# Optimization experiments

Measured on AMD Instinct MI355X. Metric: run time of the kernel, lower is better.

The kernel has to match this reference:

```python
import jax, jax.numpy as jnp
import numpy as np

EPS = 1e-5

def _rmsnorm(x, w):
    # Faithful to the repo's rms_norm: divides by sqrt(SUM of squares + eps)
    # (the .mean(-1) in the original acts on a size-1 dim and is a no-op).
    rms = jnp.sqrt(jnp.sum(x * x, axis=-1, keepdims=True) + EPS)
    return (x / rms) * w

def _conv2d(x, w, b):
    # x: (N, C=m, H=L, W=2*d_model), w: (O, I, 3, 3), padding=1 -> SAME
    y = jax.lax.conv_general_dilated(
        x, w, window_strides=(1, 1), padding='SAME',
        dimension_numbers=('NCHW', 'OIHW', 'NCHW'))
    return y + b[None, :, None, None]

def _ssm(x, fc1_W, fc1_b, fc2_W, fc2_b, A):
    # x: (b, m, l, d) with d = 2*d_model; state dim n = 128
    Bm = x @ fc2_W.T + fc2_b                       # (b,m,l,n); C = fc2(x) as well -> identical
    delta = jax.nn.softplus(x @ fc1_W.T + fc1_b)   # (b,m,l,d)
    dA = jnp.exp(jnp.einsum('bmld,dn->bmldn', delta, A))   # (b,m,l,d,n)
    dB = jnp.einsum('bmld,bmln->bmldn', delta, Bm)         # (b,m,l,d,n)
    h_new = dA + x[..., None] * dB                 # h is initialized to ones and never updated
    return jnp.einsum('bmln,bmldn->bmld', Bm, h_new)

def setup_inputs() -> dict:
    key = jax.random.key(0)
    ks = jax.random.split(key, 16)
    B, M, L, D = 1, 2, 256, 256
    D2, S = 2 * D, 128
    def rn(k, shape, scale=0.02):
        return jax.random.normal(k, shape, jnp.float32) * scale
    return {
        'x': jax.random.normal(ks[0], (B, M, L, D), jnp.float32),
        'mouth': jax.random.normal(ks[1], (B, M, L, D), jnp.float32),
        'norm_w': jnp.ones((D,), jnp.float32),
        'inp_W': rn(ks[2], (D2, D)), 'inp_b': rn(ks[3], (D2,)),
        'out_W': rn(ks[4], (D, D2)), 'out_b': jnp.ones((D,), jnp.float32),  # bias init 1.0
        'Dlin_W': rn(ks[5], (D2, D)), 'Dlin_b': rn(ks[6], (D2,)),
        'conv_W': rn(ks[7], (M, M, 3, 3), 0.1), 'conv_b': rn(ks[8], (M,)),
        'fc1_W': rn(ks[9], (D2, D2)), 'fc1_b': rn(ks[10], (D2,)),
        'fc2_W': rn(ks[11], (S, D2)), 'fc2_b': rn(ks[12], (S,)),
        'A': rn(ks[13], (D2, S), 0.05),
    }

def reference(x, mouth, norm_w, inp_W, inp_b, out_W, out_b, Dlin_W, Dlin_b,
              conv_W, conv_b, fc1_W, fc1_b, fc2_W, fc2_b, A):
    x_n = _rmsnorm(x, norm_w)
    m_n = _rmsnorm(mouth, norm_w)
    x_p = x_n @ inp_W.T + inp_b        # (B,M,L,2D)
    m_p = m_n @ inp_W.T + inp_b
    x_c = jax.nn.silu(_conv2d(x_p, conv_W, conv_b))
    m_c = jax.nn.silu(_conv2d(m_p, conv_W, conv_b))
    x_s = jax.nn.silu(_ssm(x_c, fc1_W, fc1_b, fc2_W, fc2_b, A))
    m_s = jax.nn.silu(_ssm(m_c, fc1_W, fc1_b, fc2_W, fc2_b, A))
    res = jax.nn.silu(x_n @ Dlin_W.T + Dlin_b)   # D(x) uses the normed x
    comb = x_s * res + m_s * res
    return comb @ out_W.T + out_b
```

## Files before the change

### kernel.cpp

```cpp
#include <hip/hip_runtime.h>
#include <hip/hip_bf16.h>
#include <math.h>


#define D_   256
#define D2_  512
#define S_   128

__device__ __forceinline__ float silu_f(float v) {
    return v / (1.f + __expf(-v));
}
__device__ __forceinline__ float softplus_f(float v) {
    return fmaxf(v, 0.f) + log1pf(__expf(-fabsf(v)));
}

template<bool NORM, int ACT1, int ACT2>
__global__ __launch_bounds__(256) void gemm_dual_k(
        const float* __restrict__ A0, const float* __restrict__ A1,
        const float* __restrict__ nw,
        const float* __restrict__ W1, const float* __restrict__ bias1,
        float* __restrict__ O1, int nct1, int ldo1, int n1,
        const float* __restrict__ W2, const float* __restrict__ bias2,
        float* __restrict__ O2, int nct2, int ldo2, int K) {
    __shared__ float As[2][32][36];
    __shared__ float Ws[2][32][68];
    const int b = blockIdx.x;
    const float *W, *bias; float* O; int ldo, act, rt, ct;
    if (b < n1) { W = W1; bias = bias1; O = O1; ldo = ldo1; act = ACT1; rt = b / nct1; ct = b % nct1; }
    else { int bb = b - n1; W = W2; bias = bias2; O = O2; ldo = ldo2; act = ACT2; rt = bb / nct2; ct = bb % nct2; }
    const int r0 = rt * 32, c0 = ct * 64;
    const int t = threadIdx.x;
    const int sr = t >> 3;
    const int sk = (t & 7) << 2;
    const int rowA = r0 + sr;
    const float* rowbase = (rowA < 512) ? (A0 + (size_t)rowA * K)
                                        : (A1 + (size_t)(rowA - 512) * K);
    float ascale = 1.f;
    if (NORM) {
        const int j = t & 7;
        float ssum = 0.f;
        const float* rp = rowbase + j * 32;
#pragma unroll
        for (int q = 0; q < 8; ++q) {
            float4 v = *(const float4*)(rp + q * 4);
            ssum += v.x * v.x + v.y * v.y + v.z * v.z + v.w * v.w;
        }
        ssum += __shfl_xor(ssum, 1);
        ssum += __shfl_xor(ssum, 2);
        ssum += __shfl_xor(ssum, 4);
        ascale = 1.f / sqrtf(ssum + 1e-5f);
    }
    const float* Abase  = rowbase + sk;
    const float* W1base = W + (size_t)(c0 + sr) * K + sk;
    const float* W2base = W + (size_t)(c0 + 32 + sr) * K + sk;
    float4 areg  = *(const float4*)Abase;
    float4 w1reg = *(const float4*)W1base;
    float4 w2reg = *(const float4*)W2base;
    float4 nwreg = NORM ? *(const float4*)(nw + sk) : make_float4(0.f, 0.f, 0.f, 0.f);
    const int tr = (t >> 5) << 2;
    const int tc = (t & 31) << 1;
    float acc[4][2] = {};
    const int nch = K >> 5;
    for (int ch = 0; ch < nch; ++ch) {
        const int p = ch & 1;
        float4 a = areg;
        if (NORM) {
            a.x *= ascale * nwreg.x; a.y *= ascale * nwreg.y;
            a.z *= ascale * nwreg.z; a.w *= ascale * nwreg.w;
        }
        As[p][sk + 0][sr] = a.x;  As[p][sk + 1][sr] = a.y;
        As[p][sk + 2][sr] = a.z;  As[p][sk + 3][sr] = a.w;
        Ws[p][sk + 0][sr] = w1reg.x;  Ws[p][sk + 1][sr] = w1reg.y;
        Ws[p][sk + 2][sr] = w1reg.z;  Ws[p][sk + 3][sr] = w1reg.w;
        Ws[p][sk + 0][sr + 32] = w2reg.x;  Ws[p][sk + 1][sr + 32] = w2reg.y;
        Ws[p][sk + 2][sr + 32] = w2reg.z;  Ws[p][sk + 3][sr + 32] = w2reg.w;
        __syncthreads();
        if (ch + 1 < nch) {
            const int ko = (ch + 1) << 5;
            areg  = *(const float4*)(Abase + ko);
            w1reg = *(const float4*)(W1base + ko);
            w2reg = *(const float4*)(W2base + ko);
            if (NORM) nwreg = *(const float4*)(nw + ko + sk);
        }
#pragma unroll
        for (int kk = 0; kk < 32; ++kk) {
            const float4 a4 = *(const float4*)&As[p][kk][tr];
            const float2 w2 = *(const float2*)&Ws[p][kk][tc];
            acc[0][0] = fmaf(a4.x, w2.x, acc[0][0]); acc[0][1] = fmaf(a4.x, w2.y, acc[0][1]);
            acc[1][0] = fmaf(a4.y, w2.x, acc[1][0]); acc[1][1] = fmaf(a4.y, w2.y, acc[1][1]);
            acc[2][0] = fmaf(a4.z, w2.x, acc[2][0]); acc[2][1] = fmaf(a4.z, w2.y, acc[2][1]);
            acc[3][0] = fmaf(a4.w, w2.x, acc[3][0]); acc[3][1] = fmaf(a4.w, w2.y, acc[3][1]);
        }
    }
    const float2 bv = *(const float2*)(bias + c0 + tc);
#pragma unroll
    for (int i = 0; i < 4; ++i) {
        float vx = acc[i][0] + bv.x, vy = acc[i][1] + bv.y;
        if (act == 1)      { vx = silu_f(vx);     vy = silu_f(vy); }
        else if (act == 2) { vx = softplus_f(vx); vy = softplus_f(vy); }
        *(float2*)(O + (size_t)(r0 + tr + i) * ldo + c0 + tc) = make_float2(vx, vy);
    }
}

__global__ void conv_silu_k(const float* __restrict__ xp, const float* __restrict__ cW,
                            const float* __restrict__ cb, float* __restrict__ xc) {
    int idx = blockIdx.x * blockDim.x + threadIdx.x;
    int w = idx & 511;
    int l = (idx >> 9) & 255;
    int o = (idx >> 17) & 1;
    int t = idx >> 18;
    float acc = cb[o];
#pragma unroll
    for (int i = 0; i < 2; ++i) {
        const float* base = xp + (size_t)((t * 2 + i) * 256) * 512;
#pragma unroll
        for (int dh = -1; dh <= 1; ++dh) {
            int ll = l + dh;
            if (ll < 0 || ll > 255) continue;
#pragma unroll
            for (int dw = -1; dw <= 1; ++dw) {
                int ww = w + dw;
                if (ww < 0 || ww > 511) continue;
                acc += base[(size_t)ll * 512 + ww] * cW[((o * 2 + i) * 3 + (dh + 1)) * 3 + (dw + 1)];
            }
        }
    }
    xc[idx] = silu_f(acc);
}

__global__ __launch_bounds__(512) void ssm_out_k(
        const float* __restrict__ xc, const float* __restrict__ delta,
        const float* __restrict__ Bm, const float* __restrict__ A,
        const float* __restrict__ res, const float* __restrict__ outW,
        const float* __restrict__ outb, float* __restrict__ out) {
    __shared__ float Bms[2][2][S_];
    __shared__ float combs[2][D2_];
    __shared__ float red[8];
    const int tid = threadIdx.x;
    const int m  = blockIdx.x >> 7;
    const int l0 = (blockIdx.x & 127) << 1;

    {
        const int g = tid >> 7;
        const int tt = g >> 1, lr = g & 1, n = tid & 127;
        const int rg = tt * 512 + m * 256 + l0 + lr;
        float bv = Bm[(size_t)rg * S_ + n];
        Bms[tt][lr][n] = bv;
        float sq = bv * bv;
        for (int off = 32; off; off >>= 1) sq += __shfl_xor(sq, off);
        if ((tid & 63) == 0) red[tid >> 6] = sq;
    }
    __syncthreads();
    {
        const int d = tid;
        float s2[2][2];
#pragma unroll
        for (int g = 0; g < 4; ++g) s2[g >> 1][g & 1] = red[2 * g] + red[2 * g + 1];
        float dl[2][2], xcv[2][2], rsv[2];
#pragma unroll
        for (int tt = 0; tt < 2; ++tt)
#pragma unroll
            for (int lr = 0; lr < 2; ++lr) {
                const size_t r = (size_t)(tt * 512 + m * 256 + l0 + lr);
                dl[tt][lr]  = delta[r * D2_ + d];
                xcv[tt][lr] = xc[r * D2_ + d];
            }
        rsv[0] = res[(size_t)(m * 256 + l0) * D2_ + d];
        rsv[1] = res[(size_t)(m * 256 + l0 + 1) * D2_ + d];
        float accs[2][2] = {};
        const float4* arow = (const float4*)(A + (size_t)d * S_);
        for (int k4 = 0; k4 < 32; ++k4) {
            float4 a4 = arow[k4];
            const int n = k4 * 4;
#pragma unroll
            for (int cmp = 0; cmp < 4; ++cmp) {
                float a = (cmp == 0) ? a4.x : (cmp == 1) ? a4.y : (cmp == 2) ? a4.z : a4.w;
#pragma unroll
                for (int tt = 0; tt < 2; ++tt)
#pragma unroll
                    for (int lr = 0; lr < 2; ++lr)
                        accs[tt][lr] += Bms[tt][lr][n + cmp] * __expf(dl[tt][lr] * a);
            }
        }
#pragma unroll
        for (int lr = 0; lr < 2; ++lr) {
            float sx = accs[0][lr] + xcv[0][lr] * dl[0][lr] * s2[0][lr];
            float sm = accs[1][lr] + xcv[1][lr] * dl[1][lr] * s2[1][lr];
            combs[lr][d] = (silu_f(sx) + silu_f(sm)) * rsv[lr];
        }
    }
    __syncthreads();
    {
        const int wv = tid >> 6, lane = tid & 63;
        const int j = lane & 15, cg = lane >> 4;
#pragma unroll
        for (int rnd = 0; rnd < 8; ++rnd) {
            const int c = wv * 32 + rnd * 4 + cg;
            const float4* wrow = (const float4*)(outW + (size_t)c * D2_);
            float a0 = 0.f, a1 = 0.f;
#pragma unroll
            for (int it = 0; it < 8; ++it) {
                const int k = it * 64 + j * 4;
                float4 w4 = wrow[it * 16 + j];
                a0 += w4.x * combs[0][k] + w4.y * combs[0][k + 1]
                    + w4.z * combs[0][k + 2] + w4.w * combs[0][k + 3];
                a1 += w4.x * combs[1][k] + w4.y * combs[1][k + 1]
                    + w4.z * combs[1][k + 2] + w4.w * combs[1][k + 3];
            }
            a0 += __shfl_xor(a0, 1); a0 += __shfl_xor(a0, 2);
            a0 += __shfl_xor(a0, 4); a0 += __shfl_xor(a0, 8);
            a1 += __shfl_xor(a1, 1); a1 += __shfl_xor(a1, 2);
            a1 += __shfl_xor(a1, 4); a1 += __shfl_xor(a1, 8);
            if (j == 0) {
                const float b = outb[c];
                out[(size_t)(m * 256 + l0)     * D_ + c] = a0 + b;
                out[(size_t)(m * 256 + l0 + 1) * D_ + c] = a1 + b;
            }
        }
    }
}

extern "C" void kernel_launch(void* const* d_in, const int* in_sizes, int n_in,
                              void* d_out, int out_size, void* d_ws, size_t ws_size,
                              hipStream_t stream) {
    const float* x      = (const float*)d_in[0];
    const float* mouth  = (const float*)d_in[1];
    const float* norm_w = (const float*)d_in[2];
    const float* inp_W  = (const float*)d_in[3];
    const float* inp_b  = (const float*)d_in[4];
    const float* out_W  = (const float*)d_in[5];
    const float* out_b  = (const float*)d_in[6];
    const float* Dlin_W = (const float*)d_in[7];
    const float* Dlin_b = (const float*)d_in[8];
    const float* conv_W = (const float*)d_in[9];
    const float* conv_b = (const float*)d_in[10];
    const float* fc1_W  = (const float*)d_in[11];
    const float* fc1_b  = (const float*)d_in[12];
    const float* fc2_W  = (const float*)d_in[13];
    const float* fc2_b  = (const float*)d_in[14];
    const float* A      = (const float*)d_in[15];

    float* ws    = (float*)d_ws;
    float* xp    = ws;
    float* xc    = xp + 1024 * 512;
    float* res   = xc + 1024 * 512;
    float* Bmb   = res + 512 * 512;
    float* delta = xp;
    float* out   = (float*)d_out;

    gemm_dual_k<true, 0, 1><<<384, 256, 0, stream>>>(
        x, mouth, norm_w,
        inp_W, inp_b, xp, 8, 512, 256,
        Dlin_W, Dlin_b, res, 8, 512, 256);
    conv_silu_k<<<2048, 256, 0, stream>>>(xp, conv_W, conv_b, xc);
    gemm_dual_k<false, 2, 0><<<320, 256, 0, stream>>>(
        xc, xc + (size_t)512 * 512, nullptr,
        fc1_W, fc1_b, delta, 8, 512, 256,
        fc2_W, fc2_b, Bmb, 2, 128, 512);
    ssm_out_k<<<256, 512, 0, stream>>>(xc, delta, Bmb, A, res,
                                       out_W, out_b, out);
}
```

Measured before the change: 161.1 us.

## Merge four kernel launches into one cooperative persistent kernel with grid syncs

```diff
diff --git a/kernel.cpp b/kernel.cpp
--- a/kernel.cpp
+++ b/kernel.cpp
@@ -1,11 +1,10 @@
 #include <hip/hip_runtime.h>
+#include <hip/hip_cooperative_groups.h>
 #include <hip/hip_bf16.h>
 #include <math.h>
 
-
-#define D_   256
-#define D2_  512
-#define S_   128
+namespace cg = cooperative_groups;
+
 
 __device__ __forceinline__ float silu_f(float v) {
     return v / (1.f + __expf(-v));
@@ -14,22 +13,13 @@
     return fmaxf(v, 0.f) + log1pf(__expf(-fabsf(v)));
 }
 
-template<bool NORM, int ACT1, int ACT2>
-__global__ __launch_bounds__(256) void gemm_dual_k(
-        const float* __restrict__ A0, const float* __restrict__ A1,
-        const float* __restrict__ nw,
-        const float* __restrict__ W1, const float* __restrict__ bias1,
-        float* __restrict__ O1, int nct1, int ldo1, int n1,
-        const float* __restrict__ W2, const float* __restrict__ bias2,
-        float* __restrict__ O2, int nct2, int ldo2, int K) {
-    __shared__ float As[2][32][36];
-    __shared__ float Ws[2][32][68];
-    const int b = blockIdx.x;
-    const float *W, *bias; float* O; int ldo, act, rt, ct;
-    if (b < n1) { W = W1; bias = bias1; O = O1; ldo = ldo1; act = ACT1; rt = b / nct1; ct = b % nct1; }
-    else { int bb = b - n1; W = W2; bias = bias2; O = O2; ldo = ldo2; act = ACT2; rt = bb / nct2; ct = bb % nct2; }
+__device__ void gemm_tile(const float* __restrict__ A0, const float* __restrict__ A1,
+                          const float* __restrict__ nw, bool NORM,
+                          const float* __restrict__ W, const float* __restrict__ bias,
+                          float* __restrict__ O, int ldo, int act,
+                          int rt, int ct, int K,
+                          float* AsB, float* WsB, int t, bool active) {
     const int r0 = rt * 32, c0 = ct * 64;
-    const int t = threadIdx.x;
     const int sr = t >> 3;
     const int sk = (t & 7) << 2;
     const int rowA = r0 + sr;
@@ -37,9 +27,8 @@
                                         : (A1 + (size_t)(rowA - 512) * K);
     float ascale = 1.f;
     if (NORM) {
-        const int j = t & 7;
         float ssum = 0.f;
-        const float* rp = rowbase + j * 32;
+        const float* rp = rowbase + (t & 7) * 32;
 #pragma unroll
         for (int q = 0; q < 8; ++q) {
             float4 v = *(const float4*)(rp + q * 4);
@@ -50,12 +39,12 @@
         ssum += __shfl_xor(ssum, 4);
         ascale = 1.f / sqrtf(ssum + 1e-5f);
     }
-    const float* Abase  = rowbase + sk;
-    const float* W1base = W + (size_t)(c0 + sr) * K + sk;
-    const float* W2base = W + (size_t)(c0 + 32 + sr) * K + sk;
-    float4 areg  = *(const float4*)Abase;
-    float4 w1reg = *(const float4*)W1base;
-    float4 w2reg = *(const float4*)W2base;
+    const float* Abase = rowbase + sk;
+    const float* W1b = W + (size_t)(c0 + sr) * K + sk;
+    const float* W2b = W + (size_t)(c0 + 32 + sr) * K + sk;
+    float4 areg = *(const float4*)Abase;
+    float4 w1   = *(const float4*)W1b;
+    float4 w2   = *(const float4*)W2b;
     float4 nwreg = NORM ? *(const float4*)(nw + sk) : make_float4(0.f, 0.f, 0.f, 0.f);
     const int tr = (t >> 5) << 2;
     const int tc = (t & 31) << 1;
@@ -68,153 +57,205 @@
             a.x *= ascale * nwreg.x; a.y *= ascale * nwreg.y;
             a.z *= ascale * nwreg.z; a.w *= ascale * nwreg.w;
         }
-        As[p][sk + 0][sr] = a.x;  As[p][sk + 1][sr] = a.y;
-        As[p][sk + 2][sr] = a.z;  As[p][sk + 3][sr] = a.w;
-        Ws[p][sk + 0][sr] = w1reg.x;  Ws[p][sk + 1][sr] = w1reg.y;
-        Ws[p][sk + 2][sr] = w1reg.z;  Ws[p][sk + 3][sr] = w1reg.w;
-        Ws[p][sk + 0][sr + 32] = w2reg.x;  Ws[p][sk + 1][sr + 32] = w2reg.y;
-        Ws[p][sk + 2][sr + 32] = w2reg.z;  Ws[p][sk + 3][sr + 32] = w2reg.w;
+        AsB[p * 1152 + (sk + 0) * 36 + sr] = a.x;
+        AsB[p * 1152 + (sk + 1) * 36 + sr] = a.y;
+        AsB[p * 1152 + (sk + 2) * 36 + sr] = a.z;
+        AsB[p * 1152 + (sk + 3) * 36 + sr] = a.w;
+        WsB[p * 2176 + (sk + 0) * 68 + sr] = w1.x;
+        WsB[p * 2176 + (sk + 1) * 68 + sr] = w1.y;
+        WsB[p * 2176 + (sk + 2) * 68 + sr] = w1.z;
+        WsB[p * 2176 + (sk + 3) * 68 + sr] = w1.w;
+        WsB[p * 2176 + (sk + 0) * 68 + sr + 32] = w2.x;
+        WsB[p * 2176 + (sk + 1) * 68 + sr + 32] = w2.y;
+        WsB[p * 2176 + (sk + 2) * 68 + sr + 32] = w2.z;
+        WsB[p * 2176 + (sk + 3) * 68 + sr + 32] = w2.w;
         __syncthreads();
         if (ch + 1 < nch) {
             const int ko = (ch + 1) << 5;
-            areg  = *(const float4*)(Abase + ko);
-            w1reg = *(const float4*)(W1base + ko);
-            w2reg = *(const float4*)(W2base + ko);
+            areg = *(const float4*)(Abase + ko);
+            w1   = *(const float4*)(W1b + ko);
+            w2   = *(const float4*)(W2b + ko);
             if (NORM) nwreg = *(const float4*)(nw + ko + sk);
         }
 #pragma unroll
         for (int kk = 0; kk < 32; ++kk) {
-            const float4 a4 = *(const float4*)&As[p][kk][tr];
-            const float2 w2 = *(const float2*)&Ws[p][kk][tc];
-            acc[0][0] = fmaf(a4.x, w2.x, acc[0][0]); acc[0][1] = fmaf(a4.x, w2.y, acc[0][1]);
-            acc[1][0] = fmaf(a4.y, w2.x, acc[1][0]); acc[1][1] = fmaf(a4.y, w2.y, acc[1][1]);
-            acc[2][0] = fmaf(a4.z, w2.x, acc[2][0]); acc[2][1] = fmaf(a4.z, w2.y, acc[2][1]);
-            acc[3][0] = fmaf(a4.w, w2.x, acc[3][0]); acc[3][1] = fmaf(a4.w, w2.y, acc[3][1]);
-        }
-    }
-    const float2 bv = *(const float2*)(bias + c0 + tc);
-#pragma unroll
-    for (int i = 0; i < 4; ++i) {
-        float vx = acc[i][0] + bv.x, vy = acc[i][1] + bv.y;
-        if (act == 1)      { vx = silu_f(vx);     vy = silu_f(vy); }
-        else if (act == 2) { vx = softplus_f(vx); vy = softplus_f(vy); }
-        *(float2*)(O + (size_t)(r0 + tr + i) * ldo + c0 + tc) = make_float2(vx, vy);
-    }
-}
-
-__global__ void conv_silu_k(const float* __restrict__ xp, const float* __restrict__ cW,
-                            const float* __restrict__ cb, float* __restrict__ xc) {
-    int idx = blockIdx.x * blockDim.x + threadIdx.x;
-    int w = idx & 511;
-    int l = (idx >> 9) & 255;
-    int o = (idx >> 17) & 1;
-    int t = idx >> 18;
-    float acc = cb[o];
-#pragma unroll
-    for (int i = 0; i < 2; ++i) {
-        const float* base = xp + (size_t)((t * 2 + i) * 256) * 512;
-#pragma unroll
-        for (int dh = -1; dh <= 1; ++dh) {
-            int ll = l + dh;
-            if (ll < 0 || ll > 255) continue;
-#pragma unroll
-            for (int dw = -1; dw <= 1; ++dw) {
-                int ww = w + dw;
-                if (ww < 0 || ww > 511) continue;
-                acc += base[(size_t)ll * 512 + ww] * cW[((o * 2 + i) * 3 + (dh + 1)) * 3 + (dw + 1)];
+            const float4 a4 = *(const float4*)&AsB[p * 1152 + kk * 36 + tr];
+            const float2 wv = *(const float2*)&WsB[p * 2176 + kk * 68 + tc];
+            acc[0][0] = fmaf(a4.x, wv.x, acc[0][0]); acc[0][1] = fmaf(a4.x, wv.y, acc[0][1]);
+            acc[1][0] = fmaf(a4.y, wv.x, acc[1][0]); acc[1][1] = fmaf(a4.y, wv.y, acc[1][1]);
+            acc[2][0] = fmaf(a4.z, wv.x, acc[2][0]); acc[2][1] = fmaf(a4.z, wv.y, acc[2][1]);
+            acc[3][0] = fmaf(a4.w, wv.x, acc[3][0]); acc[3][1] = fmaf(a4.w, wv.y, acc[3][1]);
+        }
+    }
+    if (active) {
+        const float2 bv = *(const float2*)(bias + c0 + tc);
+#pragma unroll
+        for (int i = 0; i < 4; ++i) {
+            float vx = acc[i][0] + bv.x, vy = acc[i][1] + bv.y;
+            if (act == 1)      { vx = silu_f(vx);     vy = silu_f(vy); }
+            else if (act == 2) { vx = softplus_f(vx); vy = softplus_f(vy); }
+            *(float2*)(O + (size_t)(r0 + tr + i) * ldo + c0 + tc) = make_float2(vx, vy);
+        }
+    }
+}
+
+__global__ __launch_bounds__(512) void coop_k(
+        const float* __restrict__ x, const float* __restrict__ mouth,
+        const float* __restrict__ nw,
+        const float* __restrict__ inpW, const float* __restrict__ inpb,
+        const float* __restrict__ outW, const float* __restrict__ outb,
+        const float* __restrict__ DW,   const float* __restrict__ Db,
+        const float* __restrict__ convW, const float* __restrict__ convB,
+        const float* __restrict__ fc1W, const float* __restrict__ fc1b,
+        const float* __restrict__ fc2W, const float* __restrict__ fc2b,
+        const float* __restrict__ A,
+        float* xp, float* xc, float* res, float* Bm, float* out) {
+    __shared__ float smem[13312];
+    cg::grid_group grid = cg::this_grid();
+    const int tid  = threadIdx.x;
+    const int half = tid >> 8;
+    const int t    = tid & 255;
+    float* AsB = smem + half * 6656;
+    float* WsB = AsB + 2304;
+
+    {
+        const int job = blockIdx.x * 2 + half;
+        const bool active = job < 384;
+        const int j = active ? job : 0;
+        const bool isres = j >= 256;
+        const int jj = isres ? j - 256 : j;
+        gemm_tile(x, mouth, nw, true,
+                  isres ? DW : inpW, isres ? Db : inpb,
+                  isres ? res : xp, 512, isres ? 1 : 0,
+                  jj >> 3, jj & 7, 256, AsB, WsB, t, active);
+    }
+    grid.sync();
+    {
+#pragma unroll
+        for (int jj = 0; jj < 4; ++jj) {
+            const int idx = jj * 131072 + blockIdx.x * 512 + tid;
+            const int w = idx & 511;
+            const int l = (idx >> 9) & 255;
+            const int o = (idx >> 17) & 1;
+            const int tt = idx >> 18;
+            float acc = convB[o];
+#pragma unroll
+            for (int i = 0; i < 2; ++i) {
+                const float* base = xp + (size_t)((tt * 2 + i) * 256) * 512;
+#pragma unroll
+                for (int dh = -1; dh <= 1; ++dh) {
+                    int ll = l + dh;
+                    if (ll < 0 || ll > 255) continue;
+#pragma unroll
+                    for (int dw = -1; dw <= 1; ++dw) {
+                        int ww = w + dw;
+                        if (ww < 0 || ww > 511) continue;
+                        acc += base[(size_t)ll * 512 + ww]
+                             * convW[((o * 2 + i) * 3 + (dh + 1)) * 3 + (dw + 1)];
+                    }
+                }
             }
-        }
-    }
-    xc[idx] = silu_f(acc);
-}
-
-__global__ __launch_bounds__(512) void ssm_out_k(
-        const float* __restrict__ xc, const float* __restrict__ delta,
-        const float* __restrict__ Bm, const float* __restrict__ A,
-        const float* __restrict__ res, const float* __restrict__ outW,
-        const float* __restrict__ outb, float* __restrict__ out) {
-    __shared__ float Bms[2][2][S_];
-    __shared__ float combs[2][D2_];
-    __shared__ float red[8];
-    const int tid = threadIdx.x;
-    const int m  = blockIdx.x >> 7;
-    const int l0 = (blockIdx.x & 127) << 1;
-
+            xc[idx] = silu_f(acc);
+        }
+    }
+    grid.sync();
     {
-        const int g = tid >> 7;
-        const int tt = g >> 1, lr = g & 1, n = tid & 127;
-        const int rg = tt * 512 + m * 256 + l0 + lr;
-        float bv = Bm[(size_t)rg * S_ + n];
-        Bms[tt][lr][n] = bv;
-        float sq = bv * bv;
-        for (int off = 32; off; off >>= 1) sq += __shfl_xor(sq, off);
-        if ((tid & 63) == 0) red[tid >> 6] = sq;
-    }
-    __syncthreads();
+        const int job = blockIdx.x * 2 + half;
+        const bool active = job < 320;
+        const int j = active ? job : 0;
+        const bool isfc2 = j >= 256;
+        const int jj = isfc2 ? j - 256 : j;
+        gemm_tile(xc, xc + (size_t)512 * 512, nullptr, false,
+                  isfc2 ? fc2W : fc1W, isfc2 ? fc2b : fc1b,
+                  isfc2 ? Bm : xp, isfc2 ? 128 : 512, isfc2 ? 0 : 2,
+                  isfc2 ? (jj >> 1) : (jj >> 3), isfc2 ? (jj & 1) : (jj & 7),
+                  512, AsB, WsB, t, active);
+    }
+    grid.sync();
     {
-        const int d = tid;
-        float s2[2][2];
-#pragma unroll
-        for (int g = 0; g < 4; ++g) s2[g >> 1][g & 1] = red[2 * g] + red[2 * g + 1];
-        float dl[2][2], xcv[2][2], rsv[2];
-#pragma unroll
-        for (int tt = 0; tt < 2; ++tt)
+        float* Bms   = smem;
+        float* combs = smem + 512;
+        float* red   = smem + 1536;
+        const float* delta = xp;
+        const int m  = blockIdx.x >> 7;
+        const int l0 = (blockIdx.x & 127) << 1;
+        {
+            const int g = tid >> 7;
+            const int tt = g >> 1, lr = g & 1, n = tid & 127;
+            const int rg = tt * 512 + m * 256 + l0 + lr;
+            float bv = Bm[(size_t)rg * 128 + n];
+            Bms[g * 128 + n] = bv;
+            float sq = bv * bv;
+            for (int off = 32; off; off >>= 1) sq += __shfl_xor(sq, off);
+            if ((tid & 63) == 0) red[tid >> 6] = sq;
+        }
+        __syncthreads();
+        {
+            const int d = tid;
+            float s2[2][2];
+#pragma unroll
+            for (int g = 0; g < 4; ++g) s2[g >> 1][g & 1] = red[2 * g] + red[2 * g + 1];
+            float dl[2][2], xcv[2][2], rsv[2];
+#pragma unroll
+            for (int tt = 0; tt < 2; ++tt)
+#pragma unroll
+                for (int lr = 0; lr < 2; ++lr) {
+                    const size_t r = (size_t)(tt * 512 + m * 256 + l0 + lr);
+                    dl[tt][lr]  = delta[r * 512 + d];
+                    xcv[tt][lr] = xc[r * 512 + d];
+                }
+            rsv[0] = res[(size_t)(m * 256 + l0) * 512 + d];
+            rsv[1] = res[(size_t)(m * 256 + l0 + 1) * 512 + d];
+            float accs[2][2] = {};
+            const float4* arow = (const float4*)(A + (size_t)d * 128);
+            for (int k4 = 0; k4 < 32; ++k4) {
+                float4 a4 = arow[k4];
+                const int n = k4 * 4;
+#pragma unroll
+                for (int cmp = 0; cmp < 4; ++cmp) {
+                    float a = (cmp == 0) ? a4.x : (cmp == 1) ? a4.y : (cmp == 2) ? a4.z : a4.w;
+#pragma unroll
+                    for (int tt = 0; tt < 2; ++tt)
+#pragma unroll
+                        for (int lr = 0; lr < 2; ++lr)
+                            accs[tt][lr] += Bms[(tt * 2 + lr) * 128 + n + cmp]
+                                          * __expf(dl[tt][lr] * a);
+                }
+            }
 #pragma unroll
             for (int lr = 0; lr < 2; ++lr) {
-                const size_t r = (size_t)(tt * 512 + m * 256 + l0 + lr);
-                dl[tt][lr]  = delta[r * D2_ + d];
-                xcv[tt][lr] = xc[r * D2_ + d];
+                float sx = accs[0][lr] + xcv[0][lr] * dl[0][lr] * s2[0][lr];
+                float sm = accs[1][lr] + xcv[1][lr] * dl[1][lr] * s2[1][lr];
+                combs[lr * 512 + d] = (silu_f(sx) + silu_f(sm)) * rsv[lr];
             }
-        rsv[0] = res[(size_t)(m * 256 + l0) * D2_ + d];
-        rsv[1] = res[(size_t)(m * 256 + l0 + 1) * D2_ + d];
-        float accs[2][2] = {};
-        const float4* arow = (const float4*)(A + (size_t)d * S_);
-        for (int k4 = 0; k4 < 32; ++k4) {
-            float4 a4 = arow[k4];
-            const int n = k4 * 4;
-#pragma unroll
-            for (int cmp = 0; cmp < 4; ++cmp) {
-                float a = (cmp == 0) ? a4.x : (cmp == 1) ? a4.y : (cmp == 2) ? a4.z : a4.w;
-#pragma unroll
-                for (int tt = 0; tt < 2; ++tt)
-#pragma unroll
-                    for (int lr = 0; lr < 2; ++lr)
-                        accs[tt][lr] += Bms[tt][lr][n + cmp] * __expf(dl[tt][lr] * a);
-            }
-        }
-#pragma unroll
-        for (int lr = 0; lr < 2; ++lr) {
-            float sx = accs[0][lr] + xcv[0][lr] * dl[0][lr] * s2[0][lr];
-            float sm = accs[1][lr] + xcv[1][lr] * dl[1][lr] * s2[1][lr];
-            combs[lr][d] = (silu_f(sx) + silu_f(sm)) * rsv[lr];
-        }
-    }
-    __syncthreads();
-    {
-        const int wv = tid >> 6, lane = tid & 63;
-        const int j = lane & 15, cg = lane >> 4;
-#pragma unroll
-        for (int rnd = 0; rnd < 8; ++rnd) {
-            const int c = wv * 32 + rnd * 4 + cg;
-            const float4* wrow = (const float4*)(outW + (size_t)c * D2_);
-            float a0 = 0.f, a1 = 0.f;
-#pragma unroll
-            for (int it = 0; it < 8; ++it) {
-                const int k = it * 64 + j * 4;
-                float4 w4 = wrow[it * 16 + j];
-                a0 += w4.x * combs[0][k] + w4.y * combs[0][k + 1]
-                    + w4.z * combs[0][k + 2] + w4.w * combs[0][k + 3];
-                a1 += w4.x * combs[1][k] + w4.y * combs[1][k + 1]
-                    + w4.z * combs[1][k + 2] + w4.w * combs[1][k + 3];
-            }
-            a0 += __shfl_xor(a0, 1); a0 += __shfl_xor(a0, 2);
-            a0 += __shfl_xor(a0, 4); a0 += __shfl_xor(a0, 8);
-            a1 += __shfl_xor(a1, 1); a1 += __shfl_xor(a1, 2);
-            a1 += __shfl_xor(a1, 4); a1 += __shfl_xor(a1, 8);
-            if (j == 0) {
-                const float b = outb[c];
-                out[(size_t)(m * 256 + l0)     * D_ + c] = a0 + b;
-                out[(size_t)(m * 256 + l0 + 1) * D_ + c] = a1 + b;
+        }
+        __syncthreads();
+        {
+            const int wv = tid >> 6, lane = tid & 63;
+            const int j = lane & 15, cg_ = lane >> 4;
+#pragma unroll
+            for (int rnd = 0; rnd < 8; ++rnd) {
+                const int c = wv * 32 + rnd * 4 + cg_;
+                const float4* wrow = (const float4*)(outW + (size_t)c * 512);
+                float a0 = 0.f, a1 = 0.f;
+#pragma unroll
+                for (int it = 0; it < 8; ++it) {
+                    const int k = it * 64 + j * 4;
+                    float4 w4 = wrow[it * 16 + j];
+                    a0 += w4.x * combs[k] + w4.y * combs[k + 1]
+                        + w4.z * combs[k + 2] + w4.w * combs[k + 3];
+                    a1 += w4.x * combs[512 + k] + w4.y * combs[512 + k + 1]
+                        + w4.z * combs[512 + k + 2] + w4.w * combs[512 + k + 3];
+                }
+                a0 += __shfl_xor(a0, 1); a0 += __shfl_xor(a0, 2);
+                a0 += __shfl_xor(a0, 4); a0 += __shfl_xor(a0, 8);
+                a1 += __shfl_xor(a1, 1); a1 += __shfl_xor(a1, 2);
+                a1 += __shfl_xor(a1, 4); a1 += __shfl_xor(a1, 8);
+                if (j == 0) {
+                    const float b = outb[c];
+                    out[(size_t)(m * 256 + l0)     * 256 + c] = a0 + b;
+                    out[(size_t)(m * 256 + l0 + 1) * 256 + c] = a1 + b;
+                }
             }
         }
     }
@@ -240,23 +281,20 @@
     const float* fc2_b  = (const float*)d_in[14];
     const float* A      = (const float*)d_in[15];
 
-    float* ws    = (float*)d_ws;
-    float* xp    = ws;
-    float* xc    = xp + 1024 * 512;
-    float* res   = xc + 1024 * 512;
-    float* Bmb   = res + 512 * 512;
-    float* delta = xp;
-    float* out   = (float*)d_out;
-
-    gemm_dual_k<true, 0, 1><<<384, 256, 0, stream>>>(
-        x, mouth, norm_w,
-        inp_W, inp_b, xp, 8, 512, 256,
-        Dlin_W, Dlin_b, res, 8, 512, 256);
-    conv_silu_k<<<2048, 256, 0, stream>>>(xp, conv_W, conv_b, xc);
-    gemm_dual_k<false, 2, 0><<<320, 256, 0, stream>>>(
-        xc, xc + (size_t)512 * 512, nullptr,
-        fc1_W, fc1_b, delta, 8, 512, 256,
-        fc2_W, fc2_b, Bmb, 2, 128, 512);
-    ssm_out_k<<<256, 512, 0, stream>>>(xc, delta, Bmb, A, res,
-                                       out_W, out_b, out);
-}
+    float* ws  = (float*)d_ws;
+    float* xp  = ws;
+    float* xc  = xp + 1024 * 512;
+    float* res = xc + 1024 * 512;
+    float* Bmb = res + 512 * 512;
+    float* out = (float*)d_out;
+
+    void* args[] = {
+        (void*)&x, (void*)&mouth, (void*)&norm_w,
+        (void*)&inp_W, (void*)&inp_b, (void*)&out_W, (void*)&out_b,
+        (void*)&Dlin_W, (void*)&Dlin_b, (void*)&conv_W, (void*)&conv_b,
+        (void*)&fc1_W, (void*)&fc1_b, (void*)&fc2_W, (void*)&fc2_b,
+        (void*)&A, (void*)&xp, (void*)&xc, (void*)&res, (void*)&Bmb, (void*)&out,
+    };
+    hipLaunchCooperativeKernel((const void*)coop_k, dim3(256), dim3(512),
+                               args, 0, stream);
+}
```

After: 333.2 us. +106.8%, slower.

## Use bf16 MFMA in projection GEMMs and vectorize conv to four outputs per thread

Applied to the files above, without the earlier changes.

```diff
diff --git a/kernel.cpp b/kernel.cpp
--- a/kernel.cpp
+++ b/kernel.cpp
@@ -7,39 +7,46 @@
 #define D2_  512
 #define S_   128
 
+typedef short  bf16x8 __attribute__((ext_vector_type(8)));
+typedef short  bf16x4 __attribute__((ext_vector_type(4)));
+typedef float  f32x4  __attribute__((ext_vector_type(4)));
+
 __device__ __forceinline__ float silu_f(float v) {
     return v / (1.f + __expf(-v));
 }
 __device__ __forceinline__ float softplus_f(float v) {
     return fmaxf(v, 0.f) + log1pf(__expf(-fabsf(v)));
 }
+__device__ __forceinline__ short f2bf(float f) {
+    __hip_bfloat16 h = __float2bfloat16(f);
+    return reinterpret_cast<short&>(h);
+}
 
 template<bool NORM, int ACT1, int ACT2>
-__global__ __launch_bounds__(256) void gemm_dual_k(
+__global__ __launch_bounds__(256) void gemm_mfma_k(
         const float* __restrict__ A0, const float* __restrict__ A1,
         const float* __restrict__ nw,
         const float* __restrict__ W1, const float* __restrict__ bias1,
         float* __restrict__ O1, int nct1, int ldo1, int n1,
         const float* __restrict__ W2, const float* __restrict__ bias2,
         float* __restrict__ O2, int nct2, int ldo2, int K) {
-    __shared__ float As[2][32][36];
-    __shared__ float Ws[2][32][68];
+    __shared__ __align__(16) short a_lds[2][32 * 56];
+    __shared__ __align__(16) short w_lds[2][64 * 56];
     const int b = blockIdx.x;
     const float *W, *bias; float* O; int ldo, act, rt, ct;
     if (b < n1) { W = W1; bias = bias1; O = O1; ldo = ldo1; act = ACT1; rt = b / nct1; ct = b % nct1; }
     else { int bb = b - n1; W = W2; bias = bias2; O = O2; ldo = ldo2; act = ACT2; rt = bb / nct2; ct = bb % nct2; }
     const int r0 = rt * 32, c0 = ct * 64;
     const int t = threadIdx.x;
-    const int sr = t >> 3;
-    const int sk = (t & 7) << 2;
+    const int sr = t >> 3, sk = (t & 7) << 2;
+    const int wc = t >> 2, wk = (t & 3) << 3;
     const int rowA = r0 + sr;
     const float* rowbase = (rowA < 512) ? (A0 + (size_t)rowA * K)
                                         : (A1 + (size_t)(rowA - 512) * K);
     float ascale = 1.f;
     if (NORM) {
-        const int j = t & 7;
         float ssum = 0.f;
-        const float* rp = rowbase + j * 32;
+        const float* rp = rowbase + (t & 7) * 32;
 #pragma unroll
         for (int q = 0; q < 8; ++q) {
             float4 v = *(const float4*)(rp + q * 4);
@@ -50,16 +57,18 @@
         ssum += __shfl_xor(ssum, 4);
         ascale = 1.f / sqrtf(ssum + 1e-5f);
     }
-    const float* Abase  = rowbase + sk;
-    const float* W1base = W + (size_t)(c0 + sr) * K + sk;
-    const float* W2base = W + (size_t)(c0 + 32 + sr) * K + sk;
-    float4 areg  = *(const float4*)Abase;
-    float4 w1reg = *(const float4*)W1base;
-    float4 w2reg = *(const float4*)W2base;
+    const float* Ag = rowbase + sk;
+    const float* Wg = W + (size_t)(c0 + wc) * K + wk;
+    float4 areg  = *(const float4*)Ag;
+    float4 wrega = *(const float4*)Wg;
+    float4 wregb = *(const float4*)(Wg + 4);
     float4 nwreg = NORM ? *(const float4*)(nw + sk) : make_float4(0.f, 0.f, 0.f, 0.f);
-    const int tr = (t >> 5) << 2;
-    const int tc = (t & 31) << 1;
-    float acc[4][2] = {};
+    const int wv = t >> 6, lane = t & 63;
+    const int aoff  = ((wv & 1) * 16 + (lane & 15)) * 56 + (lane >> 4) * 8;
+    const int boff0 = ((wv >> 1) * 32 + (lane & 15)) * 56 + (lane >> 4) * 8;
+    const int boff1 = boff0 + 16 * 56;
+    f32x4 acc0 = {0.f, 0.f, 0.f, 0.f};
+    f32x4 acc1 = {0.f, 0.f, 0.f, 0.f};
     const int nch = K >> 5;
     for (int ch = 0; ch < nch; ++ch) {
         const int p = ch & 1;
@@ -68,64 +77,73 @@
             a.x *= ascale * nwreg.x; a.y *= ascale * nwreg.y;
             a.z *= ascale * nwreg.z; a.w *= ascale * nwreg.w;
         }
-        As[p][sk + 0][sr] = a.x;  As[p][sk + 1][sr] = a.y;
-        As[p][sk + 2][sr] = a.z;  As[p][sk + 3][sr] = a.w;
-        Ws[p][sk + 0][sr] = w1reg.x;  Ws[p][sk + 1][sr] = w1reg.y;
-        Ws[p][sk + 2][sr] = w1reg.z;  Ws[p][sk + 3][sr] = w1reg.w;
-        Ws[p][sk + 0][sr + 32] = w2reg.x;  Ws[p][sk + 1][sr + 32] = w2reg.y;
-        Ws[p][sk + 2][sr + 32] = w2reg.z;  Ws[p][sk + 3][sr + 32] = w2reg.w;
+        bf16x4 av; av[0] = f2bf(a.x); av[1] = f2bf(a.y); av[2] = f2bf(a.z); av[3] = f2bf(a.w);
+        *(bf16x4*)&a_lds[p][sr * 56 + sk] = av;
+        bf16x8 wv8;
+        wv8[0] = f2bf(wrega.x); wv8[1] = f2bf(wrega.y); wv8[2] = f2bf(wrega.z); wv8[3] = f2bf(wrega.w);
+        wv8[4] = f2bf(wregb.x); wv8[5] = f2bf(wregb.y); wv8[6] = f2bf(wregb.z); wv8[7] = f2bf(wregb.w);
+        *(bf16x8*)&w_lds[p][wc * 56 + wk] = wv8;
         __syncthreads();
         if (ch + 1 < nch) {
             const int ko = (ch + 1) << 5;
-            areg  = *(const float4*)(Abase + ko);
-            w1reg = *(const float4*)(W1base + ko);
-            w2reg = *(const float4*)(W2base + ko);
+            areg  = *(const float4*)(Ag + ko);
+            wrega = *(const float4*)(Wg + ko);
+            wregb = *(const float4*)(Wg + ko + 4);
             if (NORM) nwreg = *(const float4*)(nw + ko + sk);
         }
-#pragma unroll
-        for (int kk = 0; kk < 32; ++kk) {
-            const float4 a4 = *(const float4*)&As[p][kk][tr];
-            const float2 w2 = *(const float2*)&Ws[p][kk][tc];
-            acc[0][0] = fmaf(a4.x, w2.x, acc[0][0]); acc[0][1] = fmaf(a4.x, w2.y, acc[0][1]);
-            acc[1][0] = fmaf(a4.y, w2.x, acc[1][0]); acc[1][1] = fmaf(a4.y, w2.y, acc[1][1]);
-            acc[2][0] = fmaf(a4.z, w2.x, acc[2][0]); acc[2][1] = fmaf(a4.z, w2.y, acc[2][1]);
-            acc[3][0] = fmaf(a4.w, w2.x, acc[3][0]); acc[3][1] = fmaf(a4.w, w2.y, acc[3][1]);
-        }
-    }
-    const float2 bv = *(const float2*)(bias + c0 + tc);
-#pragma unroll
-    for (int i = 0; i < 4; ++i) {
-        float vx = acc[i][0] + bv.x, vy = acc[i][1] + bv.y;
-        if (act == 1)      { vx = silu_f(vx);     vy = silu_f(vy); }
-        else if (act == 2) { vx = softplus_f(vx); vy = softplus_f(vy); }
-        *(float2*)(O + (size_t)(r0 + tr + i) * ldo + c0 + tc) = make_float2(vx, vy);
-    }
-}
-
-__global__ void conv_silu_k(const float* __restrict__ xp, const float* __restrict__ cW,
-                            const float* __restrict__ cb, float* __restrict__ xc) {
-    int idx = blockIdx.x * blockDim.x + threadIdx.x;
-    int w = idx & 511;
-    int l = (idx >> 9) & 255;
-    int o = (idx >> 17) & 1;
-    int t = idx >> 18;
-    float acc = cb[o];
-#pragma unroll
-    for (int i = 0; i < 2; ++i) {
-        const float* base = xp + (size_t)((t * 2 + i) * 256) * 512;
+        bf16x8 af  = *(const bf16x8*)&a_lds[p][aoff];
+        bf16x8 bf0 = *(const bf16x8*)&w_lds[p][boff0];
+        bf16x8 bf1 = *(const bf16x8*)&w_lds[p][boff1];
+        acc0 = __builtin_amdgcn_mfma_f32_16x16x32_bf16(af, bf0, acc0, 0, 0, 0);
+        acc1 = __builtin_amdgcn_mfma_f32_16x16x32_bf16(af, bf1, acc1, 0, 0, 0);
+    }
+    const int rowE = r0 + (wv & 1) * 16 + (lane >> 4) * 4;
+    const int colE = c0 + (wv >> 1) * 32 + (lane & 15);
+#pragma unroll
+    for (int cb = 0; cb < 2; ++cb) {
+        const f32x4 acc = cb ? acc1 : acc0;
+        const int col = colE + cb * 16;
+        const float bv = bias[col];
+#pragma unroll
+        for (int i = 0; i < 4; ++i) {
+            float v = acc[i] + bv;
+            if (act == 1)      v = silu_f(v);
+            else if (act == 2) v = softplus_f(v);
+            O[(size_t)(rowE + i) * ldo + col] = v;
+        }
+    }
+}
+
+__global__ __launch_bounds__(256) void conv_silu_k(
+        const float* __restrict__ xp, const float* __restrict__ cW,
+        const float* __restrict__ cb, float* __restrict__ xc) {
+    const int idx = blockIdx.x * 256 + threadIdx.x;
+    const int w0 = (idx & 127) * 4;
+    const int l  = (idx >> 7) & 255;
+    const int o  = (idx >> 15) & 1;
+    const int tt = idx >> 16;
+    const float cbv = cb[o];
+    float a[4] = {cbv, cbv, cbv, cbv};
+#pragma unroll
+    for (int ii = 0; ii < 2; ++ii) {
+        const float* base = xp + (size_t)((tt * 2 + ii) * 256) * 512;
 #pragma unroll
         for (int dh = -1; dh <= 1; ++dh) {
-            int ll = l + dh;
+            const int ll = l + dh;
             if (ll < 0 || ll > 255) continue;
-#pragma unroll
-            for (int dw = -1; dw <= 1; ++dw) {
-                int ww = w + dw;
-                if (ww < 0 || ww > 511) continue;
-                acc += base[(size_t)ll * 512 + ww] * cW[((o * 2 + i) * 3 + (dh + 1)) * 3 + (dw + 1)];
-            }
-        }
-    }
-    xc[idx] = silu_f(acc);
+            const float* p = base + (size_t)ll * 512 + w0;
+            float4 mid = *(const float4*)p;
+            float vm1 = (w0 > 0)   ? p[-1] : 0.f;
+            float vp4 = (w0 < 508) ? p[4]  : 0.f;
+            const float v[6] = {vm1, mid.x, mid.y, mid.z, mid.w, vp4};
+            const float* cwp = &cW[((o * 2 + ii) * 3 + (dh + 1)) * 3];
+#pragma unroll
+            for (int j = 0; j < 4; ++j)
+                a[j] += v[j] * cwp[0] + v[j + 1] * cwp[1] + v[j + 2] * cwp[2];
+        }
+    }
+    float4 r = make_float4(silu_f(a[0]), silu_f(a[1]), silu_f(a[2]), silu_f(a[3]));
+    *(float4*)(xc + (size_t)idx * 4) = r;
 }
 
 __global__ __launch_bounds__(512) void ssm_out_k(
@@ -248,12 +266,12 @@
     float* delta = xp;
     float* out   = (float*)d_out;
 
-    gemm_dual_k<true, 0, 1><<<384, 256, 0, stream>>>(
+    gemm_mfma_k<true, 0, 1><<<384, 256, 0, stream>>>(
         x, mouth, norm_w,
         inp_W, inp_b, xp, 8, 512, 256,
         Dlin_W, Dlin_b, res, 8, 512, 256);
-    conv_silu_k<<<2048, 256, 0, stream>>>(xp, conv_W, conv_b, xc);
-    gemm_dual_k<false, 2, 0><<<320, 256, 0, stream>>>(
+    conv_silu_k<<<512, 256, 0, stream>>>(xp, conv_W, conv_b, xc);
+    gemm_mfma_k<false, 2, 0><<<320, 256, 0, stream>>>(
         xc, xc + (size_t)512 * 512, nullptr,
         fc1_W, fc1_b, delta, 8, 512, 256,
         fc2_W, fc2_b, Bmb, 2, 128, 512);
```

Result: faster. 136.1 us (-15.5%).
